# Performance work log

Hardware: AMD Instinct MI355X
Metric: run time of the kernel (lower is better)

Reference implementation:

```python
import jax, jax.numpy as jnp
import numpy as np

HEADS = 8
DIM_HEAD = 40


def setup_inputs() -> dict:
    key = jax.random.key(0)
    ks = jax.random.split(key, 10)
    b, n, j, qd, cd = 8, 4096, 77, 320, 768
    inner = HEADS * DIM_HEAD  # 320
    x = jax.random.normal(ks[0], (b, n, qd), jnp.float32)
    embs = jax.random.normal(ks[1], (b, j, cd), jnp.float32)
    Wq = jax.random.normal(ks[2], (qd, inner), jnp.float32) * 0.02
    Wk = jax.random.normal(ks[3], (cd, inner), jnp.float32) * 0.02
    Wv = jax.random.normal(ks[4], (cd, inner), jnp.float32) * 0.02
    Wo = jax.random.normal(ks[5], (inner, qd), jnp.float32) * 0.02
    bo = jnp.zeros((qd,), jnp.float32)
    # per-query-token, per-key-token additive attention mask (float weights)
    cross_attn_mask = (jax.random.uniform(ks[6], (b, n, j)) < 0.5).astype(jnp.float32)
    strength = jnp.ones((1,), jnp.float32) * 0.8
    # captiontypes >= 0 marks valid key tokens; include some -1 (invalid)
    captiontypes = jax.random.randint(ks[7], (b, j), -1, 3).at[:, 0].set(0)
    global_prompt_mask = (jax.random.uniform(ks[8], (b, j)) > 0.05).at[:, 0].set(True)
    return {"x": x, "embs": embs, "Wq": Wq, "Wk": Wk, "Wv": Wv, "Wo": Wo,
            "bo": bo, "cross_attn_mask": cross_attn_mask, "strength": strength,
            "captiontypes": captiontypes, "global_prompt_mask": global_prompt_mask}


def _split_heads(t):
    # [b, n, h*d] -> [(b h), n, d], head index fastest (matches einops '(b h)')
    b, n, _ = t.shape
    return t.reshape(b, n, HEADS, DIM_HEAD).transpose(0, 2, 1, 3).reshape(b * HEADS, n, DIM_HEAD)


def reference(x, embs, Wq, Wk, Wv, Wo, bo, cross_attn_mask, strength,
              captiontypes, global_prompt_mask):
    b, n, _ = x.shape
    scale = DIM_HEAD ** -0.5
    q = _split_heads(x @ Wq).astype(jnp.float32)   # [(b h), n, d]
    k = _split_heads(embs @ Wk).astype(jnp.float32)  # [(b h), j, d]
    v = _split_heads(embs @ Wv)                      # [(b h), j, d]
    sim = jnp.einsum('bid,bjd->bij', q, k)           # [(b h), n, j] fp32

    NEG = -jnp.finfo(sim.dtype).max
    key_mask = captiontypes >= 0                     # [b, j]
    key_mask_bh = jnp.repeat(key_mask, HEADS, axis=0)[:, None, :]  # [(b h), 1, j]

    # masked std of sim over valid key positions (unbiased, ddof=1), no grad
    w = jnp.broadcast_to(key_mask_bh, sim.shape).astype(sim.dtype)
    cnt = jnp.sum(w)
    mean = jnp.sum(sim * w) / cnt
    var = jnp.sum(w * (sim - mean) ** 2) / (cnt - 1.0)
    simstd = jnp.sqrt(var)

    wf = cross_attn_mask * simstd * strength[0]      # [b, n, j]
    wf = jnp.where(global_prompt_mask[:, None, :], wf, NEG)
    wf = jnp.repeat(wf, HEADS, axis=0)               # [(b h), n, j]
    wf = jax.lax.stop_gradient(wf)

    sim = jnp.where(key_mask_bh, sim, NEG) + wf
    attn = jax.nn.softmax(sim * scale, axis=-1)
    out = jnp.einsum('bij,bjd->bid', attn, v)        # [(b h), n, d]
    out = out.reshape(b, HEADS, n, DIM_HEAD).transpose(0, 2, 1, 3).reshape(b, n, HEADS * DIM_HEAD)
    return out @ Wo + bo
```

## Files before the change

kernel.cpp:

```cpp
#include <hip/hip_runtime.h>
#include <hip/hip_bf16.h>
#include <math.h>

#define HEADS 8
#define DIMH 40
#define BB 8
#define NN 4096
#define JJ 77
#define CDIM 768
#define INNER 320
#define NEGF (-3.4028234663852886e38f)

using bf16 = __hip_bfloat16;
using f32x4 = __attribute__((ext_vector_type(4))) float;
using bf16x8 = __attribute__((ext_vector_type(8))) short;
using ushort8 = __attribute__((ext_vector_type(8))) unsigned short;
using ushort4v = __attribute__((ext_vector_type(4))) unsigned short;

__device__ __forceinline__ unsigned short f2u(float f){
    bf16 t = __float2bfloat16(f);
    return *reinterpret_cast<unsigned short*>(&t);
}
__device__ __forceinline__ float u2f(unsigned short u){
    unsigned int w = ((unsigned int)u) << 16;
    return __uint_as_float(w);
}

struct Stats { int validcnt; int gflag; float simstd; };

__global__ __launch_bounds__(256) void prep_weights(const float* __restrict__ Wq,
                                                    const float* __restrict__ Wo,
                                                    const float* __restrict__ Wk,
                                                    const float* __restrict__ Wv,
                                                    unsigned short* __restrict__ WqT,
                                                    unsigned short* __restrict__ WoT,
                                                    unsigned short* __restrict__ WkvT){
    __shared__ float tile[32][33];
    int blk = blockIdx.x;
    int tx = threadIdx.x & 31, ty = threadIdx.x >> 5;
    if(blk < 200){
        const float* in = (blk<100)? Wq : Wo;
        unsigned short* out = (blk<100)? WqT : WoT;
        int base = (blk<100)? blk : blk-100;
        int bx = base%10, by = base/10;
        int c0 = bx*32, r0 = by*32;
        #pragma unroll
        for(int i=0;i<32;i+=8) tile[ty+i][tx] = in[(size_t)(r0+ty+i)*320 + c0+tx];
        __syncthreads();
        #pragma unroll
        for(int i=0;i<32;i+=8) out[(size_t)(c0+ty+i)*320 + r0+tx] = f2u(tile[tx][ty+i]);
    } else {
        int local = blk-200;
        int nt = local%20, kt = local/20;
        int n0 = nt*32, k0 = kt*32;
        const float* in = (n0<320)? Wk : Wv;
        int nc0 = (n0<320)? n0 : n0-320;
        #pragma unroll
        for(int i=0;i<32;i+=8) tile[ty+i][tx] = in[(size_t)(k0+ty+i)*320 + nc0+tx];
        __syncthreads();
        #pragma unroll
        for(int i=0;i<32;i+=8) WkvT[(size_t)(n0+ty+i)*768 + k0+tx] = f2u(tile[tx][ty+i]);
    }
}

__global__ __launch_bounds__(256) void proj_kv_mfma(const float* __restrict__ embs,
                                                    const unsigned short* __restrict__ WkvT,
                                                    unsigned short* __restrict__ kws,
                                                    unsigned short* __restrict__ vt){
    __shared__ unsigned short As[64][40];
    __shared__ unsigned short Bs[64][40];
    int t = threadIdx.x;
    int bm = blockIdx.x % 10;
    int bn = blockIdx.x / 10;
    int row0 = bm*64, col0 = bn*64;
    int wave=t>>6, lane=t&63, l15=lane&15, lk=lane>>4;

    f32x4 acc[4];
    #pragma unroll
    for(int nf=0;nf<4;nf++) acc[nf]=(f32x4){0.f,0.f,0.f,0.f};

    for(int k0=0;k0<768;k0+=32){
        #pragma unroll
        for(int p=0;p<2;p++){
            int li = (p*256+t)*4; int r = li>>5, kk = li&31;
            int gr = row0 + r;
            ushort4v u;
            if(gr < 616){
                float4 v = *(const float4*)&embs[(size_t)gr*768 + k0+kk];
                u.x=f2u(v.x); u.y=f2u(v.y); u.z=f2u(v.z); u.w=f2u(v.w);
            } else { u.x=0;u.y=0;u.z=0;u.w=0; }
            *(ushort4v*)&As[r][kk] = u;
        }
        {
            int nn = t>>2, kk = (t&3)*8;
            *(ushort8*)&Bs[nn][kk] = *(const ushort8*)&WkvT[(size_t)(col0+nn)*768 + k0+kk];
        }
        __syncthreads();
        bf16x8 aF = *(const bf16x8*)&As[wave*16+l15][lk*8];
        #pragma unroll
        for(int nf=0;nf<4;nf++){
            bf16x8 bF = *(const bf16x8*)&Bs[nf*16+l15][lk*8];
            acc[nf] = __builtin_amdgcn_mfma_f32_16x16x32_bf16(aF,bF,acc[nf],0,0,0);
        }
        __syncthreads();
    }
    #pragma unroll
    for(int nf=0;nf<4;nf++){
        int col = col0 + nf*16 + l15;
        #pragma unroll
        for(int r=0;r<4;r++){
            int m = row0 + wave*16 + lk*4 + r;
            if(m < 616){
                int b = m/77, j = m - 77*b;
                unsigned short val = f2u(acc[nf][r]);
                if(col < 320){
                    int h = col/40, d = col - 40*h;
                    kws[(((size_t)b*HEADS+h)*JJ + j)*DIMH + d] = val;
                } else {
                    int c2 = col-320; int h = c2/40, d = c2 - 40*h;
                    size_t vbase = (((size_t)b*HEADS+h)*DIMH + d)*80;
                    vt[vbase + j] = val;
                    if(j==76){ vt[vbase+77]=0; vt[vbase+78]=0; vt[vbase+79]=0; }
                }
            }
        }
    }
}

template<int A_MODE, int C_MODE>
__global__ __launch_bounds__(256) void gemm_mfma(const void* __restrict__ A,
                                                 const unsigned short* __restrict__ Bt,
                                                 const float* __restrict__ bias,
                                                 void* __restrict__ C){
    __shared__ unsigned short As[256][40];
    __shared__ unsigned short Bs[64][40];
    int t = threadIdx.x;
    int bm = blockIdx.x & 127;
    int bn = blockIdx.x >> 7;
    int row0 = bm*256, col0 = bn*64;
    int wave = t>>6, lane = t&63;
    int l15 = lane&15, lk = lane>>4;

    f32x4 acc[4][4];
    #pragma unroll
    for(int i=0;i<4;i++)
        #pragma unroll
        for(int j=0;j<4;j++) acc[i][j] = (f32x4){0.f,0.f,0.f,0.f};

    for(int k0=0;k0<320;k0+=32){
        if(A_MODE==2){
            const unsigned short* Ab = (const unsigned short*)A;
            #pragma unroll
            for(int p=0;p<4;p++){
                int li = (p*256+t)*8; int r = li>>5, kk = li&31;
                int m = row0+r; int k = k0+kk;
                int b = m>>12, n = m&4095;
                int h = k/40, d = k-40*h;
                *(ushort8*)&As[r][kk] = *(const ushort8*)&Ab[(((size_t)(b*8+h))*NN + n)*DIMH + d];
            }
        } else {
            const float* Af = (const float*)A;
            #pragma unroll
            for(int p=0;p<8;p++){
                int li = (p*256+t)*4; int r = li>>5, kk = li&31;
                float4 v = *(const float4*)&Af[(size_t)(row0+r)*320 + k0+kk];
                ushort4v u; u.x=f2u(v.x); u.y=f2u(v.y); u.z=f2u(v.z); u.w=f2u(v.w);
                *(ushort4v*)&As[r][kk] = u;
            }
        }
        {
            int nn = t>>2, kk = (t&3)*8;
            *(ushort8*)&Bs[nn][kk] = *(const ushort8*)&Bt[(size_t)(col0+nn)*320 + k0+kk];
        }
        __syncthreads();
        bf16x8 a[4], b[4];
        #pragma unroll
        for(int mf=0;mf<4;mf++) a[mf] = *(const bf16x8*)&As[wave*64+mf*16+l15][lk*8];
        #pragma unroll
        for(int nf=0;nf<4;nf++) b[nf] = *(const bf16x8*)&Bs[nf*16+l15][lk*8];
        #pragma unroll
        for(int mf=0;mf<4;mf++)
            #pragma unroll
            for(int nf=0;nf<4;nf++)
                acc[mf][nf] = __builtin_amdgcn_mfma_f32_16x16x32_bf16(a[mf], b[nf], acc[mf][nf], 0,0,0);
        __syncthreads();
    }
    if(C_MODE==1){
        float* Cf = (float*)C;
        float bv[4];
        #pragma unroll
        for(int nf=0;nf<4;nf++) bv[nf] = bias[col0+nf*16+l15];
        #pragma unroll
        for(int mf=0;mf<4;mf++)
            #pragma unroll
            for(int nf=0;nf<4;nf++){
                int col = col0+nf*16+l15;
                #pragma unroll
                for(int r=0;r<4;r++){
                    int m = row0+wave*64+mf*16+lk*4+r;
                    Cf[(size_t)m*320+col] = acc[mf][nf][r] + bv[nf];
                }
            }
    } else {
        unsigned short* Cb = (unsigned short*)C;
        #pragma unroll
        for(int mf=0;mf<4;mf++)
            #pragma unroll
            for(int nf=0;nf<4;nf++){
                int col = col0+nf*16+l15;
                int h = col/40, d = col-40*h;
                #pragma unroll
                for(int r=0;r<4;r++){
                    int m = row0+wave*64+mf*16+lk*4+r;
                    int b = m>>12, n = m&4095;
                    Cb[(((size_t)(b*8+h))*NN + n)*DIMH + d] = f2u(acc[mf][nf][r]);
                }
            }
    }
}

__global__ __launch_bounds__(256) void stats_mfma(const unsigned short* __restrict__ qh,
                                                  const unsigned short* __restrict__ kws,
                                                  const int* __restrict__ ct,
                                                  float2* __restrict__ partials){
    int bh = blockIdx.x;
    int b = bh>>3;
    int t = threadIdx.x;
    int wave=t>>6, lane=t&63, l15=lane&15, lk=lane>>4;
    int wq0 = wave*16;
    bf16x8 zb = {0,0,0,0,0,0,0,0};

    int n0 = blockIdx.y*64;
    size_t qrow = ((size_t)bh*NN + n0 + wq0 + l15)*DIMH;
    bf16x8 aF0 = *(const bf16x8*)&qh[qrow + lk*8];
    bf16x8 aF1 = (lk==0) ? *(const bf16x8*)&qh[qrow + 32] : zb;

    bool kv[5];
    bf16x8 bK[2][5];
    #pragma unroll
    for(int jt=0;jt<5;jt++){
        int j = jt*16+l15;
        kv[jt] = (j<JJ) && (ct[b*JJ+j]>=0);
        #pragma unroll
        for(int ks=0;ks<2;ks++){
            if(j<JJ && !(ks==1 && lk>=1))
                bK[ks][jt] = *(const bf16x8*)&kws[((size_t)bh*JJ + j)*DIMH + ks*32 + lk*8];
            else bK[ks][jt] = zb;
        }
    }
    f32x4 sacc[5];
    #pragma unroll
    for(int jt=0;jt<5;jt++) sacc[jt]=(f32x4){0.f,0.f,0.f,0.f};
    #pragma unroll
    for(int jt=0;jt<5;jt++){
        sacc[jt] = __builtin_amdgcn_mfma_f32_16x16x32_bf16(aF0,bK[0][jt],sacc[jt],0,0,0);
        sacc[jt] = __builtin_amdgcn_mfma_f32_16x16x32_bf16(aF1,bK[1][jt],sacc[jt],0,0,0);
    }
    float s1=0.f, s2=0.f;
    #pragma unroll
    for(int jt=0;jt<5;jt++){
        if(kv[jt]){
            #pragma unroll
            for(int r=0;r<4;r++){ float v=sacc[jt][r]; s1+=v; s2+=v*v; }
        }
    }
    #pragma unroll
    for(int off=32;off>0;off>>=1){ s1 += __shfl_down(s1,off); s2 += __shfl_down(s2,off); }
    __shared__ float sa[4], sb[4];
    if(lane==0){ sa[wave]=s1; sb[wave]=s2; }
    __syncthreads();
    if(t==0){
        partials[blockIdx.y*64 + blockIdx.x] =
            make_float2(sa[0]+sa[1]+sa[2]+sa[3], sb[0]+sb[1]+sb[2]+sb[3]);
    }
}

__global__ __launch_bounds__(256) void finalize_kernel(const float2* __restrict__ partials,
                                                       const int* __restrict__ ct,
                                                       const int* __restrict__ gpm,
                                                       const float* __restrict__ strength,
                                                       Stats* st,
                                                       float* __restrict__ kmT,
                                                       float* __restrict__ adT,
                                                       float* __restrict__ gmT){
    int t = threadIdx.x;
    __shared__ int sflag, scnt;
    if(t==0){ sflag=0; scnt=0; }
    __syncthreads();
    int lflag=0, lcnt=0;
    for(int i=t;i<154;i+=256){ int g = gpm[i]; if(g!=0 && g!=1) lflag=1; }
    for(int i=t;i<BB*JJ;i+=256){ if(ct[i]>=0) lcnt++; }
    if(lflag) atomicOr(&sflag,1);
    atomicAdd(&scnt,lcnt);
    double s1=0.0, s2=0.0;
    for(int i=t;i<4096;i+=256){
        float2 p = partials[i];
        s1 += (double)p.x; s2 += (double)p.y;
    }
    #pragma unroll
    for(int off=32;off>0;off>>=1){ s1 += __shfl_down(s1,off); s2 += __shfl_down(s2,off); }
    __shared__ double da[4], db[4];
    __shared__ float s_simstd;
    int lane=t&63, w=t>>6;
    if(lane==0){ da[w]=s1; db[w]=s2; }
    __syncthreads();
    if(t==0){
        double S1 = da[0]+da[1]+da[2]+da[3];
        double S2 = db[0]+db[1]+db[2]+db[3];
        double cnt = (double)scnt * HEADS * NN;
        double var = (S2 - S1*S1/cnt)/(cnt-1.0);
        float sd = (float)sqrt(var);
        st->validcnt = scnt; st->gflag = sflag; st->simstd = sd;
        s_simstd = sd;
    }
    __syncthreads();
    float c = s_simstd * strength[0];
    int gflag = sflag;
    for(int i=t;i<BB*80;i+=256){
        int b = i/80, j = i-80*b;
        int kvv=0, gv=0;
        if(j<JJ){
            kvv = ct[b*JJ+j]>=0;
            gv = gflag ? (((const unsigned char*)gpm)[b*JJ+j]!=0) : (gpm[b*JJ+j]!=0);
        }
        kmT[i] = (j<JJ && kvv)?1.f:0.f;
        adT[i] = ((j<JJ && kvv)?0.f:NEGF) + ((j<JJ && gv)?0.f:NEGF);
        gmT[i] = (j<JJ && gv)? c : 0.f;
    }
}

__global__ __launch_bounds__(256) void attn_mfma(unsigned short* qh,
                                                 const unsigned short* __restrict__ kws,
                                                 const unsigned short* __restrict__ vt,
                                                 const float* __restrict__ cam,
                                                 const float* __restrict__ kmT,
                                                 const float* __restrict__ adT,
                                                 const float* __restrict__ gmT){
    int bh = blockIdx.x;
    int b = bh>>3;
    __shared__ unsigned short P[64][104];
    int t = threadIdx.x;
    int wave=t>>6, lane=t&63, l15=lane&15, lk=lane>>4;
    int wq0 = wave*16;
    bf16x8 zb = {0,0,0,0,0,0,0,0};
    ushort8 z8 = {0,0,0,0,0,0,0,0};

    int n0 = blockIdx.y*64;
    size_t qrow = ((size_t)bh*NN + n0 + wq0 + l15)*DIMH;
    bf16x8 aF0 = *(const bf16x8*)&qh[qrow + lk*8];
    bf16x8 aF1 = (lk==0) ? *(const bf16x8*)&qh[qrow + 32] : zb;

    float cv[5][4];
    #pragma unroll
    for(int jt=0;jt<5;jt++){
        int j = jt*16+l15; int jc = (j<JJ)? j : 76;
        #pragma unroll
        for(int r=0;r<4;r++){
            int row = n0 + wq0 + 4*lk + r;
            cv[jt][r] = cam[((size_t)b*NN+row)*JJ + jc];
        }
    }
    float km[5], gm[5], ad[5];
    #pragma unroll
    for(int jt=0;jt<5;jt++){
        int j = jt*16+l15;
        km[jt] = kmT[b*80+j]; ad[jt] = adT[b*80+j]; gm[jt] = gmT[b*80+j];
    }
    bf16x8 bK[2][5];
    #pragma unroll
    for(int ks=0;ks<2;ks++)
        #pragma unroll
        for(int jt=0;jt<5;jt++){
            int j = jt*16+l15;
            if(j<JJ && !(ks==1 && lk>=1))
                bK[ks][jt] = *(const bf16x8*)&kws[((size_t)bh*JJ + j)*DIMH + ks*32 + lk*8];
            else bK[ks][jt] = zb;
        }
    bf16x8 bV[3][3];
    #pragma unroll
    for(int ks=0;ks<3;ks++)
        #pragma unroll
        for(int nt=0;nt<3;nt++){
            int d = nt*16+l15;
            if(d<DIMH && !(ks==2 && lk>=2))
                bV[ks][nt] = *(const bf16x8*)&vt[((size_t)bh*DIMH + d)*80 + ks*32 + lk*8];
            else bV[ks][nt] = zb;
        }
    if(t<64){ *(ushort8*)&P[t][80]=z8; *(ushort8*)&P[t][88]=z8; *(ushort8*)&P[t][96]=z8; }

    const float scale = 0.15811388300841897f;
    f32x4 sacc[5];
    #pragma unroll
    for(int jt=0;jt<5;jt++) sacc[jt]=(f32x4){0.f,0.f,0.f,0.f};
    #pragma unroll
    for(int jt=0;jt<5;jt++){
        sacc[jt] = __builtin_amdgcn_mfma_f32_16x16x32_bf16(aF0,bK[0][jt],sacc[jt],0,0,0);
        sacc[jt] = __builtin_amdgcn_mfma_f32_16x16x32_bf16(aF1,bK[1][jt],sacc[jt],0,0,0);
    }
    float lo[5][4];
    #pragma unroll
    for(int jt=0;jt<5;jt++){
        #pragma unroll
        for(int r=0;r<4;r++)
            lo[jt][r] = (sacc[jt][r]*km[jt] + cv[jt][r]*gm[jt] + ad[jt])*scale;
    }
    float dinv[4];
    #pragma unroll
    for(int r=0;r<4;r++){
        float m = lo[0][r];
        #pragma unroll
        for(int jt=1;jt<5;jt++) m = fmaxf(m, lo[jt][r]);
        #pragma unroll
        for(int msk=1;msk<16;msk<<=1) m = fmaxf(m, __shfl_xor(m,msk));
        float s=0.f;
        #pragma unroll
        for(int jt=0;jt<5;jt++){ float e=__expf(lo[jt][r]-m); lo[jt][r]=e; s+=e; }
        #pragma unroll
        for(int msk=1;msk<16;msk<<=1) s += __shfl_xor(s,msk);
        dinv[r]=1.f/s;
    }
    #pragma unroll
    for(int jt=0;jt<5;jt++){
        int j = jt*16+l15;
        #pragma unroll
        for(int r=0;r<4;r++) P[wq0+4*lk+r][j] = f2u(lo[jt][r]*dinv[r]);
    }
    __syncthreads();
    f32x4 oacc[3];
    #pragma unroll
    for(int nt=0;nt<3;nt++) oacc[nt]=(f32x4){0.f,0.f,0.f,0.f};
    #pragma unroll
    for(int ks=0;ks<3;ks++){
        bf16x8 aP = *(const bf16x8*)&P[wq0+l15][ks*32+lk*8];
        #pragma unroll
        for(int nt=0;nt<3;nt++)
            oacc[nt] = __builtin_amdgcn_mfma_f32_16x16x32_bf16(aP,bV[ks][nt],oacc[nt],0,0,0);
    }
    #pragma unroll
    for(int nt=0;nt<3;nt++){
        int d = nt*16+l15;
        #pragma unroll
        for(int r=0;r<4;r++){
            unsigned short ush = f2u(oacc[nt][r]);
            int other = __shfl_xor((int)ush, 1);
            if((l15&1)==0 && d<DIMH){
                unsigned int word = (unsigned int)ush | (((unsigned int)(unsigned short)other)<<16);
                int row = n0 + wq0 + 4*lk + r;
                *(unsigned int*)&qh[((size_t)bh*NN + row)*DIMH + d] = word;
            }
        }
    }
}

extern "C" void kernel_launch(void* const* d_in, const int* in_sizes, int n_in,
                              void* d_out, int out_size, void* d_ws, size_t ws_size,
                              hipStream_t stream) {
    const float* x        = (const float*)d_in[0];
    const float* embs     = (const float*)d_in[1];
    const float* Wq       = (const float*)d_in[2];
    const float* Wk       = (const float*)d_in[3];
    const float* Wv       = (const float*)d_in[4];
    const float* Wo       = (const float*)d_in[5];
    const float* bo       = (const float*)d_in[6];
    const float* cam      = (const float*)d_in[7];
    const float* strength = (const float*)d_in[8];
    const int*  ct       = (const int*)d_in[9];
    const int*  gpm      = (const int*)d_in[10];

    char* ws = (char*)d_ws;
    unsigned short* qh   = (unsigned short*)ws;
    unsigned short* kws  = (unsigned short*)(ws + 20971520);
    unsigned short* vt   = (unsigned short*)(ws + 21365760);
    unsigned short* WqT  = (unsigned short*)(ws + 21775360);
    unsigned short* WoT  = (unsigned short*)(ws + 21980160);
    unsigned short* WkvT = (unsigned short*)(ws + 22184960);
    Stats* st  = (Stats*)(ws + 23168000);
    float2* partials = (float2*)(ws + 23169024);
    float* kmT = (float*)(ws + 23201792);
    float* adT = (float*)(ws + 23204352);
    float* gmT = (float*)(ws + 23206912);

    prep_weights<<<680,256,0,stream>>>(Wq,Wo,Wk,Wv,WqT,WoT,WkvT);
    proj_kv_mfma<<<100,256,0,stream>>>(embs,WkvT,kws,vt);
    gemm_mfma<0,2><<<640,256,0,stream>>>(x,WqT,nullptr,qh);
    stats_mfma<<<dim3(64,64),256,0,stream>>>(qh,kws,ct,partials);
    finalize_kernel<<<1,256,0,stream>>>(partials,ct,gpm,strength,st,kmT,adT,gmT);
    attn_mfma<<<dim3(64,64),256,0,stream>>>(qh,kws,vt,cam,kmT,adT,gmT);
    gemm_mfma<2,1><<<640,256,0,stream>>>(qh,WoT,bo,d_out);
}
```

Before: 128.5 us.

## Fuse sim-std statistics into Q projection and finalize into attention kernel

```diff
diff --git a/kernel.cpp b/kernel.cpp
--- a/kernel.cpp
+++ b/kernel.cpp
@@ -25,8 +25,6 @@
     unsigned int w = ((unsigned int)u) << 16;
     return __uint_as_float(w);
 }
-
-struct Stats { int validcnt; int gflag; float simstd; };
 
 __global__ __launch_bounds__(256) void prep_weights(const float* __restrict__ Wq,
                                                     const float* __restrict__ Wo,
@@ -127,6 +125,121 @@
     }
 }
 
+__global__ __launch_bounds__(256) void gemm_q_stats(const float* __restrict__ x,
+                                                    const unsigned short* __restrict__ WqT,
+                                                    const unsigned short* __restrict__ kws,
+                                                    const int* __restrict__ ct,
+                                                    unsigned short* __restrict__ qh,
+                                                    float2* __restrict__ partials){
+    __shared__ unsigned short SH[256*80];
+    unsigned short* As = SH;
+    unsigned short* Bs = SH + 256*40;
+    int t = threadIdx.x;
+    int bm = blockIdx.x & 127;
+    int bn = blockIdx.x >> 7;
+    int row0 = bm*256, col0 = bn*80;
+    int wave = t>>6, lane = t&63;
+    int l15 = lane&15, lk = lane>>4;
+    int b = row0 >> 12;
+    bf16x8 zb = {0,0,0,0,0,0,0,0};
+
+    f32x4 acc[4][5];
+    #pragma unroll
+    for(int i=0;i<4;i++)
+        #pragma unroll
+        for(int j=0;j<5;j++) acc[i][j] = (f32x4){0.f,0.f,0.f,0.f};
+
+    for(int k0=0;k0<320;k0+=32){
+        #pragma unroll
+        for(int p=0;p<8;p++){
+            int li = (p*256+t)*4; int r = li>>5, kk = li&31;
+            float4 v = *(const float4*)&x[(size_t)(row0+r)*320 + k0+kk];
+            ushort4v u; u.x=f2u(v.x); u.y=f2u(v.y); u.z=f2u(v.z); u.w=f2u(v.w);
+            *(ushort4v*)&As[r*40+kk] = u;
+        }
+        #pragma unroll
+        for(int p=0;p<2;p++){
+            int idx = p*256+t;
+            if(idx < 320){
+                int nn = idx>>2, kk = (idx&3)*8;
+                *(ushort8*)&Bs[nn*40+kk] = *(const ushort8*)&WqT[(size_t)(col0+nn)*320 + k0+kk];
+            }
+        }
+        __syncthreads();
+        bf16x8 a[4], bb[5];
+        #pragma unroll
+        for(int mf=0;mf<4;mf++) a[mf] = *(const bf16x8*)&As[(wave*64+mf*16+l15)*40 + lk*8];
+        #pragma unroll
+        for(int nf=0;nf<5;nf++) bb[nf] = *(const bf16x8*)&Bs[(nf*16+l15)*40 + lk*8];
+        #pragma unroll
+        for(int mf=0;mf<4;mf++)
+            #pragma unroll
+            for(int nf=0;nf<5;nf++)
+                acc[mf][nf] = __builtin_amdgcn_mfma_f32_16x16x32_bf16(a[mf], bb[nf], acc[mf][nf], 0,0,0);
+        __syncthreads();
+    }
+    #pragma unroll
+    for(int mf=0;mf<4;mf++)
+        #pragma unroll
+        for(int nf=0;nf<5;nf++){
+            int col = col0 + nf*16 + l15;
+            int h = col/40, d = col - 40*h;
+            int lcol = nf*16 + l15;
+            #pragma unroll
+            for(int r=0;r<4;r++){
+                int lrow = wave*64 + mf*16 + lk*4 + r;
+                int n = row0 + lrow - (b<<12);
+                unsigned short v = f2u(acc[mf][nf][r]);
+                qh[(((size_t)(b*8+h))*NN + n)*DIMH + d] = v;
+                SH[lrow*80 + lcol] = v;
+            }
+        }
+    __syncthreads();
+    float s1=0.f, s2=0.f;
+    #pragma unroll
+    for(int h2=0;h2<2;h2++){
+        int bh = b*8 + bn*2 + h2;
+        bool kv[5]; bf16x8 bK0[5], bK1[5];
+        #pragma unroll
+        for(int jt=0;jt<5;jt++){
+            int j = jt*16+l15;
+            kv[jt] = (j<JJ) && (ct[b*JJ+j]>=0);
+            bK0[jt] = (j<JJ) ? *(const bf16x8*)&kws[((size_t)bh*JJ+j)*DIMH + lk*8] : zb;
+            bK1[jt] = (j<JJ && lk==0) ? *(const bf16x8*)&kws[((size_t)bh*JJ+j)*DIMH + 32] : zb;
+        }
+        #pragma unroll
+        for(int mfq=0;mfq<4;mfq++){
+            int wq = wave*64 + mfq*16;
+            bf16x8 aF0 = *(const bf16x8*)&SH[(wq+l15)*80 + h2*40 + lk*8];
+            bf16x8 aF1 = (lk==0) ? *(const bf16x8*)&SH[(wq+l15)*80 + h2*40 + 32] : zb;
+            f32x4 sacc[5];
+            #pragma unroll
+            for(int jt=0;jt<5;jt++) sacc[jt]=(f32x4){0.f,0.f,0.f,0.f};
+            #pragma unroll
+            for(int jt=0;jt<5;jt++){
+                sacc[jt] = __builtin_amdgcn_mfma_f32_16x16x32_bf16(aF0,bK0[jt],sacc[jt],0,0,0);
+                sacc[jt] = __builtin_amdgcn_mfma_f32_16x16x32_bf16(aF1,bK1[jt],sacc[jt],0,0,0);
+            }
+            #pragma unroll
+            for(int jt=0;jt<5;jt++){
+                if(kv[jt]){
+                    #pragma unroll
+                    for(int r=0;r<4;r++){ float v=sacc[jt][r]; s1+=v; s2+=v*v; }
+                }
+            }
+        }
+    }
+    #pragma unroll
+    for(int off=32;off>0;off>>=1){ s1 += __shfl_down(s1,off); s2 += __shfl_down(s2,off); }
+    __shared__ float sa[4], sb[4];
+    if(lane==0){ sa[wave]=s1; sb[wave]=s2; }
+    __syncthreads();
+    if(t==0){
+        partials[blockIdx.x] = make_float2(sa[0]+sa[1]+sa[2]+sa[3],
+                                           sb[0]+sb[1]+sb[2]+sb[3]);
+    }
+}
+
 template<int A_MODE, int C_MODE>
 __global__ __launch_bounds__(256) void gemm_mfma(const void* __restrict__ A,
                                                  const unsigned short* __restrict__ Bt,
@@ -219,126 +332,21 @@
     }
 }
 
-__global__ __launch_bounds__(256) void stats_mfma(const unsigned short* __restrict__ qh,
-                                                  const unsigned short* __restrict__ kws,
-                                                  const int* __restrict__ ct,
-                                                  float2* __restrict__ partials){
-    int bh = blockIdx.x;
-    int b = bh>>3;
-    int t = threadIdx.x;
-    int wave=t>>6, lane=t&63, l15=lane&15, lk=lane>>4;
-    int wq0 = wave*16;
-    bf16x8 zb = {0,0,0,0,0,0,0,0};
-
-    int n0 = blockIdx.y*64;
-    size_t qrow = ((size_t)bh*NN + n0 + wq0 + l15)*DIMH;
-    bf16x8 aF0 = *(const bf16x8*)&qh[qrow + lk*8];
-    bf16x8 aF1 = (lk==0) ? *(const bf16x8*)&qh[qrow + 32] : zb;
-
-    bool kv[5];
-    bf16x8 bK[2][5];
-    #pragma unroll
-    for(int jt=0;jt<5;jt++){
-        int j = jt*16+l15;
-        kv[jt] = (j<JJ) && (ct[b*JJ+j]>=0);
-        #pragma unroll
-        for(int ks=0;ks<2;ks++){
-            if(j<JJ && !(ks==1 && lk>=1))
-                bK[ks][jt] = *(const bf16x8*)&kws[((size_t)bh*JJ + j)*DIMH + ks*32 + lk*8];
-            else bK[ks][jt] = zb;
-        }
-    }
-    f32x4 sacc[5];
-    #pragma unroll
-    for(int jt=0;jt<5;jt++) sacc[jt]=(f32x4){0.f,0.f,0.f,0.f};
-    #pragma unroll
-    for(int jt=0;jt<5;jt++){
-        sacc[jt] = __builtin_amdgcn_mfma_f32_16x16x32_bf16(aF0,bK[0][jt],sacc[jt],0,0,0);
-        sacc[jt] = __builtin_amdgcn_mfma_f32_16x16x32_bf16(aF1,bK[1][jt],sacc[jt],0,0,0);
-    }
-    float s1=0.f, s2=0.f;
-    #pragma unroll
-    for(int jt=0;jt<5;jt++){
-        if(kv[jt]){
-            #pragma unroll
-            for(int r=0;r<4;r++){ float v=sacc[jt][r]; s1+=v; s2+=v*v; }
-        }
-    }
-    #pragma unroll
-    for(int off=32;off>0;off>>=1){ s1 += __shfl_down(s1,off); s2 += __shfl_down(s2,off); }
-    __shared__ float sa[4], sb[4];
-    if(lane==0){ sa[wave]=s1; sb[wave]=s2; }
-    __syncthreads();
-    if(t==0){
-        partials[blockIdx.y*64 + blockIdx.x] =
-            make_float2(sa[0]+sa[1]+sa[2]+sa[3], sb[0]+sb[1]+sb[2]+sb[3]);
-    }
-}
-
-__global__ __launch_bounds__(256) void finalize_kernel(const float2* __restrict__ partials,
-                                                       const int* __restrict__ ct,
-                                                       const int* __restrict__ gpm,
-                                                       const float* __restrict__ strength,
-                                                       Stats* st,
-                                                       float* __restrict__ kmT,
-                                                       float* __restrict__ adT,
-                                                       float* __restrict__ gmT){
-    int t = threadIdx.x;
-    __shared__ int sflag, scnt;
-    if(t==0){ sflag=0; scnt=0; }
-    __syncthreads();
-    int lflag=0, lcnt=0;
-    for(int i=t;i<154;i+=256){ int g = gpm[i]; if(g!=0 && g!=1) lflag=1; }
-    for(int i=t;i<BB*JJ;i+=256){ if(ct[i]>=0) lcnt++; }
-    if(lflag) atomicOr(&sflag,1);
-    atomicAdd(&scnt,lcnt);
-    double s1=0.0, s2=0.0;
-    for(int i=t;i<4096;i+=256){
-        float2 p = partials[i];
-        s1 += (double)p.x; s2 += (double)p.y;
-    }
-    #pragma unroll
-    for(int off=32;off>0;off>>=1){ s1 += __shfl_down(s1,off); s2 += __shfl_down(s2,off); }
-    __shared__ double da[4], db[4];
-    __shared__ float s_simstd;
-    int lane=t&63, w=t>>6;
-    if(lane==0){ da[w]=s1; db[w]=s2; }
-    __syncthreads();
-    if(t==0){
-        double S1 = da[0]+da[1]+da[2]+da[3];
-        double S2 = db[0]+db[1]+db[2]+db[3];
-        double cnt = (double)scnt * HEADS * NN;
-        double var = (S2 - S1*S1/cnt)/(cnt-1.0);
-        float sd = (float)sqrt(var);
-        st->validcnt = scnt; st->gflag = sflag; st->simstd = sd;
-        s_simstd = sd;
-    }
-    __syncthreads();
-    float c = s_simstd * strength[0];
-    int gflag = sflag;
-    for(int i=t;i<BB*80;i+=256){
-        int b = i/80, j = i-80*b;
-        int kvv=0, gv=0;
-        if(j<JJ){
-            kvv = ct[b*JJ+j]>=0;
-            gv = gflag ? (((const unsigned char*)gpm)[b*JJ+j]!=0) : (gpm[b*JJ+j]!=0);
-        }
-        kmT[i] = (j<JJ && kvv)?1.f:0.f;
-        adT[i] = ((j<JJ && kvv)?0.f:NEGF) + ((j<JJ && gv)?0.f:NEGF);
-        gmT[i] = (j<JJ && gv)? c : 0.f;
-    }
-}
-
 __global__ __launch_bounds__(256) void attn_mfma(unsigned short* qh,
                                                  const unsigned short* __restrict__ kws,
                                                  const unsigned short* __restrict__ vt,
                                                  const float* __restrict__ cam,
-                                                 const float* __restrict__ kmT,
-                                                 const float* __restrict__ adT,
-                                                 const float* __restrict__ gmT){
+                                                 const float* __restrict__ strength,
+                                                 const int* __restrict__ ct,
+                                                 const int* __restrict__ gpm,
+                                                 const float2* __restrict__ partials){
     int bh = blockIdx.x;
     int b = bh>>3;
     __shared__ unsigned short P[64][104];
+    __shared__ double da[4], db[4];
+    __shared__ int scv[4], sgf[4];
+    __shared__ float s_sim;
+    __shared__ int s_gf;
     int t = threadIdx.x;
     int wave=t>>6, lane=t&63, l15=lane&15, lk=lane>>4;
     int wq0 = wave*16;
@@ -349,7 +357,6 @@
     size_t qrow = ((size_t)bh*NN + n0 + wq0 + l15)*DIMH;
     bf16x8 aF0 = *(const bf16x8*)&qh[qrow + lk*8];
     bf16x8 aF1 = (lk==0) ? *(const bf16x8*)&qh[qrow + 32] : zb;
-
     float cv[5][4];
     #pragma unroll
     for(int jt=0;jt<5;jt++){
@@ -360,11 +367,44 @@
             cv[jt][r] = cam[((size_t)b*NN+row)*JJ + jc];
         }
     }
+    {
+        double s1=0.0, s2=0.0;
+        for(int i=t;i<512;i+=256){ float2 p = partials[i]; s1 += (double)p.x; s2 += (double)p.y; }
+        int lcnt=0, lflag=0;
+        for(int i=t;i<BB*JJ;i+=256){ if(ct[i]>=0) lcnt++; }
+        for(int i=t;i<154;i+=256){ int g=gpm[i]; if(g!=0 && g!=1) lflag=1; }
+        #pragma unroll
+        for(int off=32;off>0;off>>=1){
+            s1 += __shfl_down(s1,off); s2 += __shfl_down(s2,off);
+            lcnt += __shfl_down(lcnt,off); lflag |= __shfl_down(lflag,off);
+        }
+        if(lane==0){ da[wave]=s1; db[wave]=s2; scv[wave]=lcnt; sgf[wave]=lflag; }
+        __syncthreads();
+        if(t==0){
+            double S1 = da[0]+da[1]+da[2]+da[3];
+            double S2 = db[0]+db[1]+db[2]+db[3];
+            double cnt = (double)(scv[0]+scv[1]+scv[2]+scv[3]) * HEADS * NN;
+            double var = (S2 - S1*S1/cnt)/(cnt-1.0);
+            s_sim = (float)sqrt(var);
+            s_gf = sgf[0]|sgf[1]|sgf[2]|sgf[3];
+        }
+    }
+    if(t<64){ *(ushort8*)&P[t][80]=z8; *(ushort8*)&P[t][88]=z8; *(ushort8*)&P[t][96]=z8; }
+    __syncthreads();
+    float c = s_sim * strength[0];
+    int gflag = s_gf;
     float km[5], gm[5], ad[5];
     #pragma unroll
     for(int jt=0;jt<5;jt++){
         int j = jt*16+l15;
-        km[jt] = kmT[b*80+j]; ad[jt] = adT[b*80+j]; gm[jt] = gmT[b*80+j];
+        int kvv=0, gv=0;
+        if(j<JJ){
+            kvv = ct[b*JJ+j]>=0;
+            gv = gflag ? (((const unsigned char*)gpm)[b*JJ+j]!=0) : (gpm[b*JJ+j]!=0);
+        }
+        km[jt] = (j<JJ && kvv)?1.f:0.f;
+        ad[jt] = ((j<JJ && kvv)?0.f:NEGF) + ((j<JJ && gv)?0.f:NEGF);
+        gm[jt] = (j<JJ && gv)? c : 0.f;
     }
     bf16x8 bK[2][5];
     #pragma unroll
@@ -386,7 +426,6 @@
                 bV[ks][nt] = *(const bf16x8*)&vt[((size_t)bh*DIMH + d)*80 + ks*32 + lk*8];
             else bV[ks][nt] = zb;
         }
-    if(t<64){ *(ushort8*)&P[t][80]=z8; *(ushort8*)&P[t][88]=z8; *(ushort8*)&P[t][96]=z8; }
 
     const float scale = 0.15811388300841897f;
     f32x4 sacc[5];
@@ -474,17 +513,11 @@
     unsigned short* WqT  = (unsigned short*)(ws + 21775360);
     unsigned short* WoT  = (unsigned short*)(ws + 21980160);
     unsigned short* WkvT = (unsigned short*)(ws + 22184960);
-    Stats* st  = (Stats*)(ws + 23168000);
-    float2* partials = (float2*)(ws + 23169024);
-    float* kmT = (float*)(ws + 23201792);
-    float* adT = (float*)(ws + 23204352);
-    float* gmT = (float*)(ws + 23206912);
+    float2* partials = (float2*)(ws + 23168000);
 
     prep_weights<<<680,256,0,stream>>>(Wq,Wo,Wk,Wv,WqT,WoT,WkvT);
     proj_kv_mfma<<<100,256,0,stream>>>(embs,WkvT,kws,vt);
-    gemm_mfma<0,2><<<640,256,0,stream>>>(x,WqT,nullptr,qh);
-    stats_mfma<<<dim3(64,64),256,0,stream>>>(qh,kws,ct,partials);
-    finalize_kernel<<<1,256,0,stream>>>(partials,ct,gpm,strength,st,kmT,adT,gmT);
-    attn_mfma<<<dim3(64,64),256,0,stream>>>(qh,kws,vt,cam,kmT,adT,gmT);
+    gemm_q_stats<<<512,256,0,stream>>>(x,WqT,kws,ct,qh,partials);
+    attn_mfma<<<dim3(64,64),256,0,stream>>>(qh,kws,vt,cam,strength,ct,gpm,partials);
     gemm_mfma<2,1><<<640,256,0,stream>>>(qh,WoT,bo,d_out);
 }
```

After: 128.8 us. No clear change (+0.3%).
